# Kernel tuning notes

Hardware: AMD Instinct MI355X
Metric: run time of the kernel (lower is better)

The kernel has to match this reference:

```python
import jax, jax.numpy as jnp
import numpy as np

B, N, D = 8, 4096, 3


def setup_inputs() -> dict:
    key = jax.random.key(0)
    k1, k2 = jax.random.split(key)
    array1 = jax.random.normal(k1, (B, N, D), dtype=jnp.float32)
    array2 = jax.random.normal(k2, (B, N, D), dtype=jnp.float32)
    return {"array1": array1, "array2": array2}


def reference(array1, array2):
    # Pairwise squared distances: sq[b, i, j] = ||array1[b,i] - array2[b,j]||^2
    diff = array1[:, :, None, :] - array2[:, None, :, :]   # [B, N1, N2, D]
    sq = jnp.sum(diff * diff, axis=-1)                     # [B, N1, N2]
    # array2samples_distance(a1, a2): for each point of a2, min dist to a1, then mean
    av_dist1 = jnp.mean(jnp.min(sq, axis=1), axis=-1)      # [B] (min over array1 points)
    # array2samples_distance(a2, a1): for each point of a1, min dist to a2, then mean
    av_dist2 = jnp.mean(jnp.min(sq, axis=2), axis=-1)      # [B] (min over array2 points)
    dist1 = jnp.mean(av_dist1)
    dist2 = jnp.mean(av_dist2)
    dist_all = dist1 + dist2
    return (dist_all, dist1, dist2)
```

## Files before the change

kernel.cpp:

```cpp
#include <hip/hip_runtime.h>

#define BB 8
#define NN 4096
#define THREADS 256
#define NSPLIT 32
#define CHUNK (NN / NSPLIT)
#define QPT 8
#define QPB (THREADS * QPT)
#define NQ (BB * NN)
#define NQ_TOTAL (2 * NQ)

__global__ __launch_bounds__(THREADS) void chamfer_min_kernel(
    const float* __restrict__ a1, const float* __restrict__ a2,
    float* __restrict__ minpart)
{
    __shared__ float4 sdb[CHUNK];

    const int tid = threadIdx.x;
    const int bid = blockIdx.x;
    const int c   = bid & (NSPLIT - 1);
    const int qb  = (bid >> 5) & 1;
    const int b   = (bid >> 6) & 7;
    const int dir = bid >> 9;

    const float* dbg = (dir == 0 ? a1 : a2) + (size_t)b * NN * 3;
    const float* qg  = (dir == 0 ? a2 : a1) + (size_t)b * NN * 3;

    if (tid < CHUNK) {
        const int i = c * CHUNK + tid;
        const float x = dbg[i * 3 + 0];
        const float y = dbg[i * 3 + 1];
        const float z = dbg[i * 3 + 2];
        sdb[tid] = make_float4(x, y, z, 0.5f * fmaf(x, x, fmaf(y, y, z * z)));
    }

    float qx[QPT], qy[QPT], qz[QPT];
    {
        const float4* q4 = reinterpret_cast<const float4*>(
            qg + (size_t)(qb * QPB + tid * QPT) * 3);
        const float4 v0 = q4[0], v1 = q4[1], v2 = q4[2];
        const float4 v3 = q4[3], v4 = q4[4], v5 = q4[5];
        qx[0] = -v0.x; qy[0] = -v0.y; qz[0] = -v0.z;
        qx[1] = -v0.w; qy[1] = -v1.x; qz[1] = -v1.y;
        qx[2] = -v1.z; qy[2] = -v1.w; qz[2] = -v2.x;
        qx[3] = -v2.y; qy[3] = -v2.z; qz[3] = -v2.w;
        qx[4] = -v3.x; qy[4] = -v3.y; qz[4] = -v3.z;
        qx[5] = -v3.w; qy[5] = -v4.x; qz[5] = -v4.y;
        qx[6] = -v4.z; qy[6] = -v4.w; qz[6] = -v5.x;
        qx[7] = -v5.y; qy[7] = -v5.z; qz[7] = -v5.w;
    }

    __syncthreads();

    float m[QPT];
    #pragma unroll
    for (int k = 0; k < QPT; ++k) m[k] = 3.4e38f;

    #pragma unroll 2
    for (int i = 0; i < CHUNK; i += 2) {
        const float4 p0 = sdb[i];
        const float4 p1 = sdb[i + 1];
        #pragma unroll
        for (int k = 0; k < QPT; ++k) {
            const float t0 = fmaf(p0.x, qx[k], fmaf(p0.y, qy[k], fmaf(p0.z, qz[k], p0.w)));
            const float t1 = fmaf(p1.x, qx[k], fmaf(p1.y, qy[k], fmaf(p1.z, qz[k], p1.w)));
            m[k] = fminf(fminf(t0, t1), m[k]);
        }
    }

    float4 o0, o1;
    o0.x = m[0]; o0.y = m[1]; o0.z = m[2]; o0.w = m[3];
    o1.x = m[4]; o1.y = m[5]; o1.z = m[6]; o1.w = m[7];

    const size_t qglob = (size_t)dir * NQ + (size_t)b * NN + (size_t)(qb * QPB + tid * QPT);
    float4* dst = reinterpret_cast<float4*>(minpart + (size_t)c * NQ_TOTAL + qglob);
    dst[0] = o0;
    dst[1] = o1;
}

__global__ __launch_bounds__(THREADS) void decode_sum_kernel(
    const float* __restrict__ a1, const float* __restrict__ a2,
    const float* __restrict__ minpart, float* __restrict__ partials)
{
    __shared__ float red[THREADS];
    const int tid = threadIdx.x;
    const int bid = blockIdx.x;
    const int gq  = bid * THREADS + tid;
    const int dir = gq >> 15;
    const int b   = (gq >> 12) & 7;
    const int q   = gq & (NN - 1);

    float mn = 3.4e38f;
    #pragma unroll
    for (int cc = 0; cc < NSPLIT; ++cc)
        mn = fminf(mn, minpart[(size_t)cc * NQ_TOTAL + gq]);

    const float* qp = (dir == 0 ? a2 : a1) + ((size_t)b * NN + q) * 3;
    const float qx = qp[0], qy = qp[1], qz = qp[2];
    const float qn = fmaf(qx, qx, fmaf(qy, qy, qz * qz));
    const float d  = fmaf(2.0f, mn, qn);

    red[tid] = d;
    __syncthreads();
    #pragma unroll
    for (int s = THREADS / 2; s > 0; s >>= 1) {
        if (tid < s) red[tid] += red[tid + s];
        __syncthreads();
    }
    if (tid == 0) partials[bid] = red[0];
}

__global__ __launch_bounds__(256) void finalize_kernel(
    const float* __restrict__ partials, float* __restrict__ out)
{
    __shared__ float red[256];
    const int t = threadIdx.x;
    red[t] = partials[t];
    __syncthreads();
    #pragma unroll
    for (int s = 64; s > 0; s >>= 1) {
        if ((t & 127) < s) red[t] += red[t + s];
        __syncthreads();
    }
    if (t == 0) {
        const float inv = 1.0f / (float)(BB * NN);
        const float d1 = red[0]   * inv;
        const float d2 = red[128] * inv;
        out[0] = d1 + d2;
        out[1] = d1;
        out[2] = d2;
    }
}

extern "C" void kernel_launch(void* const* d_in, const int* in_sizes, int n_in,
                              void* d_out, int out_size, void* d_ws, size_t ws_size,
                              hipStream_t stream)
{
    const float* a1 = (const float*)d_in[0];
    const float* a2 = (const float*)d_in[1];
    float* out = (float*)d_out;

    float* minpart  = (float*)d_ws;
    float* partials = (float*)((char*)d_ws + (size_t)NSPLIT * NQ_TOTAL * sizeof(float));

    hipLaunchKernelGGL(chamfer_min_kernel, dim3(2 * BB * 2 * NSPLIT), dim3(THREADS), 0, stream,
                       a1, a2, minpart);
    hipLaunchKernelGGL(decode_sum_kernel, dim3(NQ_TOTAL / THREADS), dim3(THREADS), 0, stream,
                       a1, a2, minpart, partials);
    hipLaunchKernelGGL(finalize_kernel, dim3(1), dim3(256), 0, stream,
                       partials, out);
}
```

Before: 33.95 us.

## Halve database split count and fold finalize into decode via last-block atomics

Drops the database split from 32 to 16 chunks, so each block scans 256 points and the decode pass reads half as many partial minima. It also removes the separate finalize kernel. Decode blocks now atomically add their sums into per-direction accumulators, and the last block to arrive, tracked by an atomic counter, writes the outputs. The accumulators and counter are zeroed by the first block of the min kernel. The trade-offs are half as many min-kernel blocks, which means less parallelism, and a float atomic reduction whose summation order is nondeterministic.

Result: slower. 36.80 us (+8.4%).

```diff
diff --git a/kernel.cpp b/kernel.cpp
--- a/kernel.cpp
+++ b/kernel.cpp
@@ -3,12 +3,15 @@
 #define BB 8
 #define NN 4096
 #define THREADS 256
-#define NSPLIT 32
+#define NSPLIT 16
 #define CHUNK (NN / NSPLIT)
 #define QPT 8
 #define QPB (THREADS * QPT)
 #define NQ (BB * NN)
 #define NQ_TOTAL (2 * NQ)
+#define DECODE_BLOCKS (NQ_TOTAL / THREADS)
+
+#define ACC_OFF ((size_t)NSPLIT * NQ_TOTAL)
 
 __global__ __launch_bounds__(THREADS) void chamfer_min_kernel(
     const float* __restrict__ a1, const float* __restrict__ a2,
@@ -18,15 +21,21 @@
 
     const int tid = threadIdx.x;
     const int bid = blockIdx.x;
+
+    if (bid == 0 && tid < 3) {
+        float* acc = minpart + ACC_OFF;
+        acc[tid] = 0.0f;
+    }
+
     const int c   = bid & (NSPLIT - 1);
-    const int qb  = (bid >> 5) & 1;
-    const int b   = (bid >> 6) & 7;
-    const int dir = bid >> 9;
+    const int qb  = (bid >> 4) & 1;
+    const int b   = (bid >> 5) & 7;
+    const int dir = bid >> 8;
 
     const float* dbg = (dir == 0 ? a1 : a2) + (size_t)b * NN * 3;
     const float* qg  = (dir == 0 ? a2 : a1) + (size_t)b * NN * 3;
 
-    if (tid < CHUNK) {
+    {
         const int i = c * CHUNK + tid;
         const float x = dbg[i * 3 + 0];
         const float y = dbg[i * 3 + 1];
@@ -80,7 +89,7 @@
 
 __global__ __launch_bounds__(THREADS) void decode_sum_kernel(
     const float* __restrict__ a1, const float* __restrict__ a2,
-    const float* __restrict__ minpart, float* __restrict__ partials)
+    float* __restrict__ minpart, float* __restrict__ out)
 {
     __shared__ float red[THREADS];
     const int tid = threadIdx.x;
@@ -107,28 +116,23 @@
         if (tid < s) red[tid] += red[tid + s];
         __syncthreads();
     }
-    if (tid == 0) partials[bid] = red[0];
-}
 
-__global__ __launch_bounds__(256) void finalize_kernel(
-    const float* __restrict__ partials, float* __restrict__ out)
-{
-    __shared__ float red[256];
-    const int t = threadIdx.x;
-    red[t] = partials[t];
-    __syncthreads();
-    #pragma unroll
-    for (int s = 64; s > 0; s >>= 1) {
-        if ((t & 127) < s) red[t] += red[t + s];
-        __syncthreads();
-    }
-    if (t == 0) {
-        const float inv = 1.0f / (float)(BB * NN);
-        const float d1 = red[0]   * inv;
-        const float d2 = red[128] * inv;
-        out[0] = d1 + d2;
-        out[1] = d1;
-        out[2] = d2;
+    if (tid == 0) {
+        float* acc = minpart + ACC_OFF;
+        unsigned int* counter = (unsigned int*)(acc + 2);
+        atomicAdd(&acc[dir], red[0]);
+        __threadfence();
+        const unsigned int old = atomicAdd(counter, 1u);
+        if (old == DECODE_BLOCKS - 1) {
+            const float s1 = atomicAdd(&acc[0], 0.0f);
+            const float s2 = atomicAdd(&acc[1], 0.0f);
+            const float inv = 1.0f / (float)(BB * NN);
+            const float d1 = s1 * inv;
+            const float d2 = s2 * inv;
+            out[0] = d1 + d2;
+            out[1] = d1;
+            out[2] = d2;
+        }
     }
 }
 
@@ -140,13 +144,10 @@
     const float* a2 = (const float*)d_in[1];
     float* out = (float*)d_out;
 
-    float* minpart  = (float*)d_ws;
-    float* partials = (float*)((char*)d_ws + (size_t)NSPLIT * NQ_TOTAL * sizeof(float));
+    float* minpart = (float*)d_ws;
 
     hipLaunchKernelGGL(chamfer_min_kernel, dim3(2 * BB * 2 * NSPLIT), dim3(THREADS), 0, stream,
                        a1, a2, minpart);
-    hipLaunchKernelGGL(decode_sum_kernel, dim3(NQ_TOTAL / THREADS), dim3(THREADS), 0, stream,
-                       a1, a2, minpart, partials);
-    hipLaunchKernelGGL(finalize_kernel, dim3(1), dim3(256), 0, stream,
-                       partials, out);
+    hipLaunchKernelGGL(decode_sum_kernel, dim3(DECODE_BLOCKS), dim3(THREADS), 0, stream,
+                       a1, a2, minpart, out);
 }
```
